# Kernel optimization log

Hardware: AMD Instinct MI355X
Metric: run time of the kernel (lower is better)

Reference implementation:

```python
import jax, jax.numpy as jnp
import numpy as np


def setup_inputs() -> dict:
    key = jax.random.key(0)
    k1, k2 = jax.random.split(key)
    N, F, E = 100000, 128, 600000
    x = jax.random.normal(k1, (N, F), dtype=jnp.float32)
    edge_index = jax.random.randint(k2, (2, E), 0, N, dtype=jnp.int64)
    return {"x": x, "edge_index": edge_index}


def reference(x, edge_index):
    # x: [N, F] node features; edge_index: [2, E]
    ei = edge_index.T  # [E, 2]
    N = x.shape[0]
    E = ei.shape[0]

    # Midpoint node insertion: mean of the two endpoint features per edge.
    mid = 0.5 * (x[ei[:, 0]] + x[ei[:, 1]])  # [E, F]
    new_x = jnp.concatenate([x, mid], axis=0)  # [N+E, F]

    # New node indices N .. N+E-1
    new_idx = jnp.arange(N, N + E)
    e1 = jnp.stack([ei[:, 0], new_idx], axis=1)  # src -> midpoint
    e2 = jnp.stack([new_idx, ei[:, 1]], axis=1)  # midpoint -> dst

    # Triangle edges among consecutive triples of new nodes (vectorized form
    # of the original Python loop: for i in range(N, N+E-2, 3)).
    T = -(-(E - 2) // 3) if E > 2 else 0  # ceil((E-2)/3) == number of loop iters
    i = N + 3 * jnp.arange(T)
    tri = jnp.stack([i, i + 1, i + 1, i + 2, i + 2, i], axis=1).reshape(-1, 2)  # [3T, 2]

    new_ei = jnp.concatenate([ei, e1, e2, tri], axis=0)  # [E + 2E + 3T, 2]
    return new_x, new_ei.T
```

## Files before the change

### kernel.cpp

```cpp
#include <hip/hip_runtime.h>


#define F 128
#define F4 (F / 4)

typedef float f32x4 __attribute__((ext_vector_type(4)));

__device__ __forceinline__ void nt_store4(f32x4 v, f32x4* p) {
    asm volatile("global_store_dwordx4 %0, %1, off sc0 sc1 nt"
                 :
                 : "v"(p), "v"(v)
                 : "memory");
}

__device__ __forceinline__ void nt_store1(float v, float* p) {
    asm volatile("global_store_dword %0, %1, off sc0 sc1 nt"
                 :
                 : "v"(p), "v"(v)
                 : "memory");
}

__global__ void unpool_fused_kernel(const f32x4* __restrict__ x4,
                                    const int* __restrict__ ei0,
                                    const int* __restrict__ ei1,
                                    f32x4* __restrict__ out4,
                                    float* __restrict__ r0,
                                    float* __restrict__ r1,
                                    int N, int E, int M, int EB,
                                    long long totalRows) {
    if (blockIdx.x < (unsigned)EB) {
        const int col = blockIdx.x * blockDim.x + threadIdx.x;
        if (col >= M) return;
        int a, b;
        if (col < E) {
            a = ei0[col];
            b = ei1[col];
        } else if (col < 2 * E) {
            const int e = col - E;
            a = ei0[e];
            b = N + e;
        } else if (col < 3 * E) {
            const int e = col - 2 * E;
            a = N + e;
            b = ei1[e];
        } else {
            const int j = col - 3 * E;
            const int t = j / 3;
            const int k = j - 3 * t;
            const int i = N + 3 * t;
            a = i + k;
            b = (k < 2) ? (i + k + 1) : i;
        }
        nt_store1((float)a, &r0[col]);
        nt_store1((float)b, &r1[col]);
        return;
    }

    const int lane = threadIdx.x & 31;
    const long long grp =
        (long long)(blockIdx.x - EB) * (blockDim.x >> 5) + (threadIdx.x >> 5);
    const long long row0 = grp * 2;
    if (row0 >= totalRows) return;
    const long long row1 = row0 + 1;
    const bool have1 = (row1 < totalRows);

    const bool mid0 = (row0 >= N);
    const bool mid1 = have1 && (row1 >= N);

    f32x4 a0 = 0.f, b0 = 0.f, a1 = 0.f, b1 = 0.f;
    if (mid0) {
        const int e = (int)(row0 - N);
        const int s = ei0[e];
        const int d = ei1[e];
        a0 = x4[(long long)s * F4 + lane];
        b0 = x4[(long long)d * F4 + lane];
    } else {
        a0 = x4[row0 * F4 + lane];
    }
    if (have1) {
        if (mid1) {
            const int e = (int)(row1 - N);
            const int s = ei0[e];
            const int d = ei1[e];
            a1 = x4[(long long)s * F4 + lane];
            b1 = x4[(long long)d * F4 + lane];
        } else {
            a1 = x4[row1 * F4 + lane];
        }
    }

    f32x4 v0 = mid0 ? (0.5f * (a0 + b0)) : a0;
    nt_store4(v0, &out4[row0 * F4 + lane]);

    if (have1) {
        f32x4 v1 = mid1 ? (0.5f * (a1 + b1)) : a1;
        nt_store4(v1, &out4[row1 * F4 + lane]);
    }
}

extern "C" void kernel_launch(void* const* d_in, const int* in_sizes, int n_in,
                              void* d_out, int out_size, void* d_ws, size_t ws_size,
                              hipStream_t stream) {
    const float* x = (const float*)d_in[0];
    const int* ei = (const int*)d_in[1];

    const int N = in_sizes[0] / F;
    const int E = in_sizes[1] / 2;
    const int T = (E > 2) ? (E - 2 + 2) / 3 : 0;
    const int M = 3 * E + 3 * T;

    const int* ei0 = ei;
    const int* ei1 = ei + E;

    float* out = (float*)d_out;
    float* r0 = out + (size_t)(N + E) * F;
    float* r1 = r0 + M;

    const long long rows = (long long)N + E;
    const long long groups = (rows + 1) / 2;
    const int blocksA = (int)((groups + 7) / 8);
    const int blocksB = (M + 255) / 256;

    unpool_fused_kernel<<<blocksA + blocksB, 256, 0, stream>>>(
        (const f32x4*)x, ei0, ei1, (f32x4*)out, r0, r1,
        N, E, M, blocksB, rows);
}
```

Before: 146.0 us.

## Bucket edges by source node and pin buckets to XCDs for gather locality

Result: faster. 136.1 us (-6.8%).

```diff
diff --git a/kernel.cpp b/kernel.cpp
--- a/kernel.cpp
+++ b/kernel.cpp
@@ -2,98 +2,147 @@
 
 
 #define F 128
-#define F4 (F / 4)
+#define F4 32
+#define BSHIFT 10
+#define SLOTS 8192
+#define SPB_BLOCKS (SLOTS / 16)
+#define CHUNK 2048
 
 typedef float f32x4 __attribute__((ext_vector_type(4)));
 
 __device__ __forceinline__ void nt_store4(f32x4 v, f32x4* p) {
     asm volatile("global_store_dwordx4 %0, %1, off sc0 sc1 nt"
-                 :
-                 : "v"(p), "v"(v)
-                 : "memory");
+                 :: "v"(p), "v"(v) : "memory");
+}
+__device__ __forceinline__ void nt_store1(float v, float* p) {
+    asm volatile("global_store_dword %0, %1, off sc0 sc1 nt"
+                 :: "v"(p), "v"(v) : "memory");
 }
 
-__device__ __forceinline__ void nt_store1(float v, float* p) {
-    asm volatile("global_store_dword %0, %1, off sc0 sc1 nt"
-                 :
-                 : "v"(p), "v"(v)
-                 : "memory");
+__global__ void init_kernel(int4* __restrict__ tup, int* __restrict__ cursor,
+                            int NB, int nSlots) {
+    const int i = blockIdx.x * blockDim.x + threadIdx.x;
+    if (i < nSlots) tup[i] = make_int4(0, 0, -1, 0);
+    if (blockIdx.x == 0 && threadIdx.x < NB)
+        cursor[threadIdx.x] = threadIdx.x * SLOTS;
 }
 
-__global__ void unpool_fused_kernel(const f32x4* __restrict__ x4,
-                                    const int* __restrict__ ei0,
-                                    const int* __restrict__ ei1,
-                                    f32x4* __restrict__ out4,
-                                    float* __restrict__ r0,
-                                    float* __restrict__ r1,
-                                    int N, int E, int M, int EB,
-                                    long long totalRows) {
-    if (blockIdx.x < (unsigned)EB) {
-        const int col = blockIdx.x * blockDim.x + threadIdx.x;
+__global__ __launch_bounds__(256) void scatter_kernel(
+        const int* __restrict__ ei0, const int* __restrict__ ei1,
+        int* __restrict__ cursor, int4* __restrict__ tup, int E, int NB) {
+    __shared__ int lh[128];
+    __shared__ int lbase[128];
+    const int t = threadIdx.x;
+    if (t < 128) lh[t] = 0;
+    __syncthreads();
+    const int base = blockIdx.x * CHUNK;
+    int s[8], d[8], bk[8], rk[8];
+#pragma unroll
+    for (int i = 0; i < 8; ++i) {
+        const int e = base + i * 256 + t;
+        if (e < E) {
+            s[i] = ei0[e];
+            d[i] = ei1[e];
+            bk[i] = s[i] >> BSHIFT;
+            rk[i] = atomicAdd(&lh[bk[i]], 1);
+        } else {
+            bk[i] = -1;
+        }
+    }
+    __syncthreads();
+    if (t < NB) {
+        const int c = lh[t];
+        lbase[t] = c ? atomicAdd(&cursor[t], c) : 0;
+    }
+    __syncthreads();
+#pragma unroll
+    for (int i = 0; i < 8; ++i) {
+        if (bk[i] >= 0) {
+            const int e = base + i * 256 + t;
+            const int pos = lbase[bk[i]] + rk[i];
+            if (pos < (bk[i] + 1) * SLOTS)
+                tup[pos] = make_int4(s[i], d[i], e, 0);
+        }
+    }
+}
+
+__global__ __launch_bounds__(256) void main_kernel(
+        const f32x4* __restrict__ x4,
+        const int* __restrict__ ei0, const int* __restrict__ ei1,
+        const int4* __restrict__ tup,
+        f32x4* __restrict__ out4, float* __restrict__ r0, float* __restrict__ r1,
+        int N, int E, int M, int NB, int MB, int EBlk) {
+    const unsigned b = blockIdx.x;
+
+    if (b < (unsigned)MB) {
+        const int xcd = b & 7;
+        const int seq = b >> 3;
+        const int bucket = xcd + 8 * (seq / SPB_BLOCKS);
+        if (bucket >= NB) return;
+        const int chunk = seq % SPB_BLOCKS;
+        const int slot0 = bucket * SLOTS + chunk * 16;
+        const int lane = threadIdx.x & 31;
+        const int g = threadIdx.x >> 5;
+        const int p0 = slot0 + g * 2;
+
+        const int4 t0 = tup[p0];
+        const int4 t1 = tup[p0 + 1];
+        f32x4 a0 = 0.f, b0v = 0.f, a1 = 0.f, b1v = 0.f;
+        if (t0.z >= 0) {
+            a0  = x4[t0.x * F4 + lane];
+            b0v = x4[t0.y * F4 + lane];
+        }
+        if (t1.z >= 0) {
+            a1  = x4[t1.x * F4 + lane];
+            b1v = x4[t1.y * F4 + lane];
+        }
+        if (t0.z >= 0)
+            nt_store4(0.5f * (a0 + b0v), &out4[(size_t)(N + t0.z) * F4 + lane]);
+        if (t1.z >= 0)
+            nt_store4(0.5f * (a1 + b1v), &out4[(size_t)(N + t1.z) * F4 + lane]);
+        return;
+    }
+
+    const unsigned eb = b - MB;
+    if (eb < (unsigned)EBlk) {
+        const int col = eb * 256 + threadIdx.x;
         if (col >= M) return;
-        int a, b;
+        int a, c;
         if (col < E) {
             a = ei0[col];
-            b = ei1[col];
+            c = ei1[col];
         } else if (col < 2 * E) {
             const int e = col - E;
             a = ei0[e];
-            b = N + e;
+            c = N + e;
         } else if (col < 3 * E) {
             const int e = col - 2 * E;
             a = N + e;
-            b = ei1[e];
+            c = ei1[e];
         } else {
             const int j = col - 3 * E;
-            const int t = j / 3;
-            const int k = j - 3 * t;
-            const int i = N + 3 * t;
+            const int tt = j / 3;
+            const int k = j - 3 * tt;
+            const int i = N + 3 * tt;
             a = i + k;
-            b = (k < 2) ? (i + k + 1) : i;
+            c = (k < 2) ? (i + k + 1) : i;
         }
         nt_store1((float)a, &r0[col]);
-        nt_store1((float)b, &r1[col]);
+        nt_store1((float)c, &r1[col]);
         return;
     }
 
+    const unsigned cb = eb - EBlk;
     const int lane = threadIdx.x & 31;
-    const long long grp =
-        (long long)(blockIdx.x - EB) * (blockDim.x >> 5) + (threadIdx.x >> 5);
-    const long long row0 = grp * 2;
-    if (row0 >= totalRows) return;
+    const int g = threadIdx.x >> 5;
+    const long long row0 = (long long)cb * 16 + g * 2;
+    if (row0 < N) {
+        f32x4 v0 = x4[row0 * F4 + lane];
+        nt_store4(v0, &out4[row0 * F4 + lane]);
+    }
     const long long row1 = row0 + 1;
-    const bool have1 = (row1 < totalRows);
-
-    const bool mid0 = (row0 >= N);
-    const bool mid1 = have1 && (row1 >= N);
-
-    f32x4 a0 = 0.f, b0 = 0.f, a1 = 0.f, b1 = 0.f;
-    if (mid0) {
-        const int e = (int)(row0 - N);
-        const int s = ei0[e];
-        const int d = ei1[e];
-        a0 = x4[(long long)s * F4 + lane];
-        b0 = x4[(long long)d * F4 + lane];
-    } else {
-        a0 = x4[row0 * F4 + lane];
-    }
-    if (have1) {
-        if (mid1) {
-            const int e = (int)(row1 - N);
-            const int s = ei0[e];
-            const int d = ei1[e];
-            a1 = x4[(long long)s * F4 + lane];
-            b1 = x4[(long long)d * F4 + lane];
-        } else {
-            a1 = x4[row1 * F4 + lane];
-        }
-    }
-
-    f32x4 v0 = mid0 ? (0.5f * (a0 + b0)) : a0;
-    nt_store4(v0, &out4[row0 * F4 + lane]);
-
-    if (have1) {
-        f32x4 v1 = mid1 ? (0.5f * (a1 + b1)) : a1;
+    if (row1 < N) {
+        f32x4 v1 = x4[row1 * F4 + lane];
         nt_store4(v1, &out4[row1 * F4 + lane]);
     }
 }
@@ -116,12 +165,20 @@
     float* r0 = out + (size_t)(N + E) * F;
     float* r1 = r0 + M;
 
-    const long long rows = (long long)N + E;
-    const long long groups = (rows + 1) / 2;
-    const int blocksA = (int)((groups + 7) / 8);
-    const int blocksB = (M + 255) / 256;
+    int* cursor = (int*)d_ws;
+    int4* tup = (int4*)((char*)d_ws + 4096);
 
-    unpool_fused_kernel<<<blocksA + blocksB, 256, 0, stream>>>(
-        (const f32x4*)x, ei0, ei1, (f32x4*)out, r0, r1,
-        N, E, M, blocksB, rows);
+    const int NB = (N + (1 << BSHIFT) - 1) >> BSHIFT;
+    const int NBpad = (NB + 7) & ~7;
+    const int nSlots = NB * SLOTS;
+    const int MB = NBpad * SPB_BLOCKS;
+    const int EBlk = (M + 255) / 256;
+    const int CB = (N + 15) / 16;
+
+    init_kernel<<<(nSlots + 255) / 256, 256, 0, stream>>>(tup, cursor, NB, nSlots);
+    scatter_kernel<<<(E + CHUNK - 1) / CHUNK, 256, 0, stream>>>(
+        ei0, ei1, cursor, tup, E, NB);
+    main_kernel<<<MB + EBlk + CB, 256, 0, stream>>>(
+        (const f32x4*)x, ei0, ei1, tup, (f32x4*)out, r0, r1,
+        N, E, M, NB, MB, EBlk);
 }
```
